# Kernel optimization log

Measured on AMD Instinct MI355X. Metric: run time of the kernel, lower is better.

The kernel has to match this reference:

```python
import jax, jax.numpy as jnp
import numpy as np

D_MODEL = 1024
N_HEAD = 16


def setup_inputs() -> dict:
    key = jax.random.key(0)
    kx, kw = jax.random.split(key)
    x = jax.random.normal(kx, (4, 2048, D_MODEL), dtype=jnp.float32)
    # fused QKV projection weight, torch Linear: y = x @ W.T, W: [3*d_model, d_model]
    W_qkv = jax.random.normal(kw, (3 * D_MODEL, D_MODEL), dtype=jnp.float32) * (D_MODEL ** -0.5)
    return {"x": x, "W_qkv": W_qkv}


def reference(x, W_qkv):
    B, T, C = x.shape
    hd = C // N_HEAD
    qkv = jnp.einsum('btc,fc->btf', x, W_qkv)  # [B,T,3C]
    q, k, v = jnp.split(qkv, 3, axis=-1)
    # [B, H, T, hd]
    q = q.reshape(B, T, N_HEAD, hd).transpose(0, 2, 1, 3)
    k = k.reshape(B, T, N_HEAD, hd).transpose(0, 2, 1, 3)
    v = v.reshape(B, T, N_HEAD, hd).transpose(0, 2, 1, 3)
    scale = 1.0 / jnp.sqrt(jnp.asarray(hd, dtype=x.dtype))
    scores = jnp.einsum('bhqd,bhkd->bhqk', q, k) * scale  # [B,H,T,T]
    causal = jnp.tril(jnp.ones((T, T), dtype=bool))
    scores = jnp.where(causal, scores, jnp.asarray(-jnp.inf, dtype=scores.dtype))
    w = jax.nn.softmax(scores, axis=-1)
    out = jnp.einsum('bhqk,bhkd->bhqd', w, v)  # [B,H,T,hd]
    return out
```

## Files before the change

kernel.cpp:

```cpp
#include <hip/hip_runtime.h>
#include <hip/hip_bf16.h>
#include <math.h>

#define D_MODEL 1024
#define N_HEAD  16
#define HD      64
#define B_SZ    4
#define T_SEQ   2048
#define M_TOT   (B_SZ * T_SEQ)
#define N_TOT   (3 * D_MODEL)

typedef __bf16 bf16_t;
typedef __bf16 bf16x8 __attribute__((ext_vector_type(8)));
typedef __bf16 bf16x4 __attribute__((ext_vector_type(4)));
typedef __bf16 bf16x2 __attribute__((ext_vector_type(2)));
typedef float  f32x4  __attribute__((ext_vector_type(4)));
typedef float  f32x16 __attribute__((ext_vector_type(16)));
typedef int    i32x4  __attribute__((ext_vector_type(4)));

#define Q_PRESCALE 0.18033688011112042f

__global__ __launch_bounds__(256) void cvt_f32_bf16(const float* __restrict__ in,
                                                    bf16_t* __restrict__ out, int n4) {
  int i = blockIdx.x * blockDim.x + threadIdx.x;
  int stride = gridDim.x * blockDim.x;
  for (; i < n4; i += stride) {
    float4 v = ((const float4*)in)[i];
    bf16x4 o;
    o[0] = (bf16_t)v.x; o[1] = (bf16_t)v.y; o[2] = (bf16_t)v.z; o[3] = (bf16_t)v.w;
    ((bf16x4*)out)[i] = o;
  }
}

__global__ __launch_bounds__(256) void qkv_gemm(const bf16_t* __restrict__ xb,
                                                const bf16_t* __restrict__ wb,
                                                bf16_t* __restrict__ Q,
                                                bf16_t* __restrict__ Kf,
                                                bf16_t* __restrict__ Vf) {
  __shared__ alignas(16) bf16_t smem[24576];
  bf16_t* a_lds = smem;
  bf16_t* b_lds = smem + 12288;
  bf16_t* c_lds = smem;

  const int tid  = threadIdx.x;
  const int wave = tid >> 6;
  const int lane = tid & 63;
  const int bm = blockIdx.y * 128;
  const int bn = blockIdx.x * 128;
  const int sec = bn >> 10;

  f32x4 acc[4][4] = {};

  const int sRow  = lane >> 2;
  const int sCol8 = (lane & 3) ^ ((lane >> 3) & 3);
  const int fr = lane & 15;
  const int fk = lane >> 4;
  const int wm = (wave >> 1) * 64;
  const int wn = (wave & 1) * 64;

  auto stage = [&](int buf, int kk) {
#pragma unroll
    for (int c = 0; c < 2; ++c) {
      const int chunk = wave * 2 + c;
      const bf16_t* gA = &xb[(size_t)(bm + chunk * 16 + sRow) * D_MODEL + kk + sCol8 * 8];
      __builtin_amdgcn_global_load_lds(
          (__attribute__((address_space(1))) void*)(void*)gA,
          (__attribute__((address_space(3))) void*)&a_lds[buf * 4096 + chunk * 512], 16, 0, 0);
      const bf16_t* gB = &wb[(size_t)(bn + chunk * 16 + sRow) * D_MODEL + kk + sCol8 * 8];
      __builtin_amdgcn_global_load_lds(
          (__attribute__((address_space(1))) void*)(void*)gB,
          (__attribute__((address_space(3))) void*)&b_lds[buf * 4096 + chunk * 512], 16, 0, 0);
    }
  };

  auto loadFrags = [&](int buf, bf16x8 af[4], bf16x8 bfr[4]) {
#pragma unroll
    for (int mt = 0; mt < 4; ++mt) {
      const int row = wm + mt * 16 + fr;
      af[mt] = *(const bf16x8*)&a_lds[buf * 4096 + row * 32 + (fk ^ ((fr >> 1) & 3)) * 8];
    }
#pragma unroll
    for (int nt = 0; nt < 4; ++nt) {
      const int row = wn + nt * 16 + fr;
      bfr[nt] = *(const bf16x8*)&b_lds[buf * 4096 + row * 32 + (fk ^ ((fr >> 1) & 3)) * 8];
    }
  };

  auto mfmaAll = [&](bf16x8 af[4], bf16x8 bfr[4]) {
    __builtin_amdgcn_s_setprio(1);
#pragma unroll
    for (int mt = 0; mt < 4; ++mt)
#pragma unroll
      for (int nt = 0; nt < 4; ++nt)
        acc[mt][nt] = __builtin_amdgcn_mfma_f32_16x16x32_bf16(af[mt], bfr[nt], acc[mt][nt], 0, 0, 0);
    __builtin_amdgcn_s_setprio(0);
  };

  stage(0, 0);
  stage(1, 32);
  int cur = 0;
  for (int t = 0; t < 31; ++t) {
    asm volatile("s_waitcnt vmcnt(4)" ::: "memory");
    __builtin_amdgcn_s_barrier();
    __builtin_amdgcn_sched_barrier(0);
    bf16x8 af[4], bfr[4];
    loadFrags(cur, af, bfr);
    if (t < 30) stage((t + 2) % 3, (t + 2) * 32);
    mfmaAll(af, bfr);
    cur = (cur + 1) % 3;
  }
  asm volatile("s_waitcnt vmcnt(0)" ::: "memory");
  __builtin_amdgcn_s_barrier();
  __builtin_amdgcn_sched_barrier(0);
  {
    bf16x8 af[4], bfr[4];
    loadFrags(cur, af, bfr);
    mfmaAll(af, bfr);
  }

  const int cRowBase = (lane >> 4) * 4;
  const int cCol     = lane & 15;

  if (sec == 2) {
#pragma unroll
    for (int mt = 0; mt < 4; ++mt) {
#pragma unroll
      for (int nt = 0; nt < 4; ++nt) {
        const int hn = (bn & 1023) + wn + nt * 16 + cCol;
        const int h  = hn >> 6;
        const int d  = hn & 63;
        const int mbase = bm + wm + mt * 16 + cRowBase;
        const int b  = mbase >> 11;
        const int t0 = mbase & 2047;
        const int kvt = t0 >> 5, tt0 = t0 & 31;
        const int idx = (d >> 5) * 2 + (tt0 >> 4);
        const int h2  = (tt0 >> 3) & 1;
        const int j0  = tt0 & 7;
        bf16x4 pk;
        pk[0] = (bf16_t)acc[mt][nt][0]; pk[1] = (bf16_t)acc[mt][nt][1];
        pk[2] = (bf16_t)acc[mt][nt][2]; pk[3] = (bf16_t)acc[mt][nt][3];
        const size_t bhOff = (size_t)(b * N_HEAD + h) * (T_SEQ * HD);
        *(bf16x4*)&Vf[bhOff + (size_t)(((kvt * 4 + idx) * 64 + h2 * 32 + (d & 31)) * 8 + j0)] = pk;
      }
    }
  } else {
    __syncthreads();
    const float qs = (sec == 0) ? Q_PRESCALE : 1.0f;
#pragma unroll
    for (int mt = 0; mt < 4; ++mt)
#pragma unroll
      for (int nt = 0; nt < 4; ++nt)
#pragma unroll
        for (int r = 0; r < 4; ++r) {
          const int mloc = wm + mt * 16 + cRowBase + r;
          const int nloc = wn + nt * 16 + cCol;
          c_lds[mloc * 132 + nloc] = (bf16_t)(acc[mt][nt][r] * qs);
        }
    __syncthreads();

    const int row = tid >> 1;
    const int nh  = tid & 1;
    const int m = bm + row;
    const int b = m >> 11, t = m & 2047;
    const int h = ((bn & 1023) + nh * 64) >> 6;
    const size_t bhOff = (size_t)(b * N_HEAD + h) * (T_SEQ * HD);

    if (sec == 0) {
      bf16_t* qp = Q + bhOff + (size_t)t * HD;
#pragma unroll
      for (int o = 0; o < 16; ++o) {
        bf16x4 vv = *(const bf16x4*)&c_lds[row * 132 + nh * 64 + o * 4];
        *(bf16x4*)&qp[o * 4] = vv;
      }
    } else {
      const int kvt = t >> 5, lk = t & 31;
#pragma unroll
      for (int o = 0; o < 16; ++o) {
        const int d0 = o * 4;
        const int cc = d0 >> 4, h2 = (d0 >> 3) & 1, j0 = d0 & 7;
        bf16x4 vv = *(const bf16x4*)&c_lds[row * 132 + nh * 64 + d0];
        *(bf16x4*)&Kf[bhOff + (size_t)(((kvt * 4 + cc) * 64 + h2 * 32 + lk) * 8 + j0)] = vv;
      }
    }
  }
}

__device__ inline int pack_bf16(float lo, float hi) {
  bf16x2 v; v[0] = (bf16_t)lo; v[1] = (bf16_t)hi;
  return __builtin_bit_cast(int, v);
}
__device__ inline void permswap(int& a, int& b) {
  asm volatile("v_permlane32_swap_b32 %0, %1" : "+v"(a), "+v"(b));
}
__device__ inline void loadK4(bf16x8 k[4], const bf16_t* __restrict__ Kbase,
                              int kv0, int lane) {
  const bf16_t* p = Kbase + (size_t)(kv0 >> 5) * 2048 + lane * 8;
#pragma unroll
  for (int c = 0; c < 4; ++c) k[c] = *(const bf16x8*)(p + c * 512);
}
__device__ inline void loadV4(bf16x8 v[4], const bf16_t* __restrict__ Vbase,
                              int kv0, int lane) {
  const bf16_t* p = Vbase + (size_t)(kv0 >> 5) * 2048 + lane * 8;
#pragma unroll
  for (int idx = 0; idx < 4; ++idx) v[idx] = *(const bf16x8*)(p + idx * 512);
}

__global__ __launch_bounds__(256, 4) void attn_fwd(const bf16_t* __restrict__ Q,
                                                   const bf16_t* __restrict__ Kf,
                                                   const bf16_t* __restrict__ Vf,
                                                   float* __restrict__ out) {
  __shared__ float o_sh[2][64][33];
  __shared__ float m_sh[2][32];
  __shared__ float l_sh[2][32];

  const int tid  = threadIdx.x;
  const int wave = tid >> 6;
  const int lane = tid & 63;
  const int l31  = lane & 31;
  const int hi   = lane >> 5;

  const int f   = blockIdx.x;
  const int bh  = ((f & 7) << 3) | ((f >> 3) & 7);
  const int pr  = f >> 6;
  const int grp = wave >> 1;
  const int isWriter = wave & 1;
  const int chunk = grp ? (63 - pr) : pr;
  const int q0 = chunk * 32;
  const int n  = chunk + 1;
  const int h  = (n + 1) >> 1;
  const int j0 = isWriter ? h : 0;
  const int j1 = isWriter ? n : h;

  const bf16_t* Qp = Q  + (size_t)bh * T_SEQ * HD;
  const bf16_t* Kp = Kf + (size_t)bh * T_SEQ * HD;
  const bf16_t* Vp = Vf + (size_t)bh * T_SEQ * HD;
  float* op = out + (size_t)bh * T_SEQ * HD;

  bf16x8 qf[4];
#pragma unroll
  for (int c = 0; c < 4; ++c)
    qf[c] = *(const bf16x8*)&Qp[(size_t)(q0 + l31) * HD + c * 16 + hi * 8];

  f32x16 o0 = {}, o1 = {};
  float m_run = -INFINITY;
  float l_run = 0.f;

  if (j0 < j1) {
    bf16x8 kA[4], vA[4];
    loadK4(kA, Kp, j0 * 32, lane);

    for (int j = j0; j < j1; ++j) {
      const int kv0 = j * 32;
      loadV4(vA, Vp, kv0, lane);

      f32x16 st = {};
      __builtin_amdgcn_s_setprio(1);
#pragma unroll
      for (int c = 0; c < 4; ++c)
        st = __builtin_amdgcn_mfma_f32_32x32x16_bf16(kA[c], qf[c], st, 0, 0, 0);
      __builtin_amdgcn_s_setprio(0);

      const int nxt = (j + 1 < j1) ? (j + 1) * 32 : kv0;
      loadK4(kA, Kp, nxt, lane);

      if (kv0 == q0) {
#pragma unroll
        for (int r = 0; r < 16; ++r) {
          const int koff = (r & 3) + 8 * (r >> 2) + 4 * hi;
          st[r] = (koff > l31) ? -INFINITY : st[r];
        }
      }
      float pm = fmaxf(fmaxf(fmaxf(st[0], st[1]), fmaxf(st[2], st[3])),
                       fmaxf(fmaxf(st[4], st[5]), fmaxf(st[6], st[7])));
      pm = fmaxf(pm, fmaxf(fmaxf(fmaxf(st[8], st[9]), fmaxf(st[10], st[11])),
                           fmaxf(fmaxf(st[12], st[13]), fmaxf(st[14], st[15]))));

      if (__any(!(pm <= m_run + 8.f))) {
        const float pm_full = fmaxf(pm, __shfl_xor(pm, 32));
        const float m_new = fmaxf(m_run, pm_full);
        const float alpha = exp2f(m_run - m_new);
        m_run = m_new;
        l_run *= alpha;
#pragma unroll
        for (int r = 0; r < 16; ++r) {
          const int qr = (r & 3) + 8 * (r >> 2) + 4 * hi;
          const float av = __shfl(alpha, qr);
          o0[r] *= av; o1[r] *= av;
        }
      }

      float p[16];
#pragma unroll
      for (int r = 0; r < 16; ++r) p[r] = exp2f(st[r] - m_run);
      float s0 = (p[0] + p[1]) + (p[2] + p[3]);
      float s1 = (p[4] + p[5]) + (p[6] + p[7]);
      float s2 = (p[8] + p[9]) + (p[10] + p[11]);
      float s3 = (p[12] + p[13]) + (p[14] + p[15]);
      l_run += (s0 + s1) + (s2 + s3);

      int a01 = pack_bf16(p[0],  p[1]),  a23 = pack_bf16(p[2],  p[3]);
      int b01 = pack_bf16(p[4],  p[5]),  b23 = pack_bf16(p[6],  p[7]);
      int c01 = pack_bf16(p[8],  p[9]),  c23 = pack_bf16(p[10], p[11]);
      int d01 = pack_bf16(p[12], p[13]), d23 = pack_bf16(p[14], p[15]);
      permswap(a01, b01); permswap(a23, b23);
      permswap(c01, d01); permswap(c23, d23);
      i32x4 w1 = {a01, a23, b01, b23};
      i32x4 w2 = {c01, c23, d01, d23};
      bf16x8 f1 = __builtin_bit_cast(bf16x8, w1);
      bf16x8 f2 = __builtin_bit_cast(bf16x8, w2);

      __builtin_amdgcn_s_setprio(1);
      o0 = __builtin_amdgcn_mfma_f32_32x32x16_bf16(f1, vA[0], o0, 0, 0, 0);
      o0 = __builtin_amdgcn_mfma_f32_32x32x16_bf16(f2, vA[1], o0, 0, 0, 0);
      o1 = __builtin_amdgcn_mfma_f32_32x32x16_bf16(f1, vA[2], o1, 0, 0, 0);
      o1 = __builtin_amdgcn_mfma_f32_32x32x16_bf16(f2, vA[3], o1, 0, 0, 0);
      __builtin_amdgcn_s_setprio(0);
    }
  }

  const float l_comb = l_run + __shfl_xor(l_run, 32);

  if (isWriter) {
#pragma unroll
    for (int r = 0; r < 16; ++r) {
      o_sh[grp][lane][r]      = o0[r];
      o_sh[grp][lane][16 + r] = o1[r];
    }
    if (lane < 32) {
      m_sh[grp][lane] = m_run;
      l_sh[grp][lane] = l_comb;
    }
  }
  __syncthreads();
  if (!isWriter) {
#pragma unroll
    for (int r = 0; r < 16; ++r) {
      const int qr = (r & 3) + 8 * (r >> 2) + 4 * hi;
      const float mB = m_sh[grp][qr];
      const float lB = l_sh[grp][qr];
      const float mA = __shfl(m_run, qr);
      const float lA = __shfl(l_comb, qr);
      const float mM = fmaxf(mA, mB);
      const float aA = exp2f(mA - mM);
      const float aB = exp2f(mB - mM);
      const float li = 1.f / (lA * aA + lB * aB);
      const float x0 = (o0[r] * aA + o_sh[grp][lane][r]      * aB) * li;
      const float x1 = (o1[r] * aA + o_sh[grp][lane][16 + r] * aB) * li;
      op[(size_t)(q0 + qr) * HD + l31]      = x0;
      op[(size_t)(q0 + qr) * HD + 32 + l31] = x1;
    }
  }
}

extern "C" void kernel_launch(void* const* d_in, const int* in_sizes, int n_in,
                              void* d_out, int out_size, void* d_ws, size_t ws_size,
                              hipStream_t stream) {
  const float* x = (const float*)d_in[0];
  const float* W = (const float*)d_in[1];
  float* out = (float*)d_out;

  char* ws = (char*)d_ws;
  bf16_t* xb  = (bf16_t*)(ws);
  bf16_t* wb  = (bf16_t*)(ws + 16777216);
  bf16_t* Qb  = (bf16_t*)(ws + 16777216 + 6291456);
  bf16_t* Kfb = Qb + 8388608;
  bf16_t* Vfb = Kfb + 8388608;

  cvt_f32_bf16<<<2048, 256, 0, stream>>>(x, xb, (M_TOT * D_MODEL) / 4);
  cvt_f32_bf16<<<1024, 256, 0, stream>>>(W, wb, (N_TOT * D_MODEL) / 4);

  dim3 ggrid(N_TOT / 128, M_TOT / 128);
  qkv_gemm<<<ggrid, 256, 0, stream>>>(xb, wb, Qb, Kfb, Vfb);

  attn_fwd<<<2048, 256, 0, stream>>>(Qb, Kfb, Vfb, out);
}
```

Measured before the change: 151.3 us.

## Split each query chunk's KV range across four waves instead of pairing chunks

Each attention block previously took two mirrored query chunks (pr and 63-pr), and two waves split each chunk's KV range in half. Now each block handles a single query chunk, and all four waves each take a quarter of the KV tiles. Wave 0 merges the other three waves' partial outputs using the online-softmax rescaling, and the grid doubles to 4096 blocks. This is meant to shorten each wave's serial KV loop and rely on the block scheduler for load balance. In exchange it adds a larger four-way LDS reduction, leaves waves idle on short early chunks, and drops the explicit pairing that balanced work per block.

```diff
diff --git a/kernel.cpp b/kernel.cpp
--- a/kernel.cpp
+++ b/kernel.cpp
@@ -209,9 +209,9 @@
                                                    const bf16_t* __restrict__ Kf,
                                                    const bf16_t* __restrict__ Vf,
                                                    float* __restrict__ out) {
-  __shared__ float o_sh[2][64][33];
-  __shared__ float m_sh[2][32];
-  __shared__ float l_sh[2][32];
+  __shared__ float o_sh[3][64][33];
+  __shared__ float m_sh[3][32];
+  __shared__ float l_sh[3][32];
 
   const int tid  = threadIdx.x;
   const int wave = tid >> 6;
@@ -219,17 +219,14 @@
   const int l31  = lane & 31;
   const int hi   = lane >> 5;
 
-  const int f   = blockIdx.x;
-  const int bh  = ((f & 7) << 3) | ((f >> 3) & 7);
-  const int pr  = f >> 6;
-  const int grp = wave >> 1;
-  const int isWriter = wave & 1;
-  const int chunk = grp ? (63 - pr) : pr;
+  const int f     = blockIdx.x;
+  const int bh    = ((f & 7) << 3) | ((f >> 3) & 7);
+  const int chunk = f >> 6;
   const int q0 = chunk * 32;
   const int n  = chunk + 1;
-  const int h  = (n + 1) >> 1;
-  const int j0 = isWriter ? h : 0;
-  const int j1 = isWriter ? n : h;
+  const int s  = (n + 3) >> 2;
+  const int j0 = wave * s;
+  const int j1 = min(j0 + s, n);
 
   const bf16_t* Qp = Q  + (size_t)bh * T_SEQ * HD;
   const bf16_t* Kp = Kf + (size_t)bh * T_SEQ * HD;
@@ -320,32 +317,35 @@
 
   const float l_comb = l_run + __shfl_xor(l_run, 32);
 
-  if (isWriter) {
+  if (wave != 0) {
+    const int slot = wave - 1;
 #pragma unroll
     for (int r = 0; r < 16; ++r) {
-      o_sh[grp][lane][r]      = o0[r];
-      o_sh[grp][lane][16 + r] = o1[r];
+      o_sh[slot][lane][r]      = o0[r];
+      o_sh[slot][lane][16 + r] = o1[r];
     }
     if (lane < 32) {
-      m_sh[grp][lane] = m_run;
-      l_sh[grp][lane] = l_comb;
+      m_sh[slot][lane] = m_run;
+      l_sh[slot][lane] = l_comb;
     }
   }
   __syncthreads();
-  if (!isWriter) {
+  if (wave == 0) {
 #pragma unroll
     for (int r = 0; r < 16; ++r) {
       const int qr = (r & 3) + 8 * (r >> 2) + 4 * hi;
-      const float mB = m_sh[grp][qr];
-      const float lB = l_sh[grp][qr];
       const float mA = __shfl(m_run, qr);
       const float lA = __shfl(l_comb, qr);
-      const float mM = fmaxf(mA, mB);
-      const float aA = exp2f(mA - mM);
-      const float aB = exp2f(mB - mM);
-      const float li = 1.f / (lA * aA + lB * aB);
-      const float x0 = (o0[r] * aA + o_sh[grp][lane][r]      * aB) * li;
-      const float x1 = (o1[r] * aA + o_sh[grp][lane][16 + r] * aB) * li;
+      const float m1 = m_sh[0][qr], m2 = m_sh[1][qr], m3 = m_sh[2][qr];
+      const float l1 = l_sh[0][qr], l2 = l_sh[1][qr], l3 = l_sh[2][qr];
+      const float mM = fmaxf(fmaxf(mA, m1), fmaxf(m2, m3));
+      const float a0 = exp2f(mA - mM), a1 = exp2f(m1 - mM);
+      const float a2 = exp2f(m2 - mM), a3 = exp2f(m3 - mM);
+      const float li = 1.f / (lA * a0 + l1 * a1 + l2 * a2 + l3 * a3);
+      const float x0 = (o0[r] * a0 + o_sh[0][lane][r] * a1 +
+                        o_sh[1][lane][r] * a2 + o_sh[2][lane][r] * a3) * li;
+      const float x1 = (o1[r] * a0 + o_sh[0][lane][16 + r] * a1 +
+                        o_sh[1][lane][16 + r] * a2 + o_sh[2][lane][16 + r] * a3) * li;
       op[(size_t)(q0 + qr) * HD + l31]      = x0;
       op[(size_t)(q0 + qr) * HD + 32 + l31] = x1;
     }
@@ -372,5 +372,5 @@
   dim3 ggrid(N_TOT / 128, M_TOT / 128);
   qkv_gemm<<<ggrid, 256, 0, stream>>>(xb, wb, Qb, Kfb, Vfb);
 
-  attn_fwd<<<2048, 256, 0, stream>>>(Qb, Kfb, Vfb, out);
-}
+  attn_fwd<<<4096, 256, 0, stream>>>(Qb, Kfb, Vfb, out);
+}
```

After: 154.8 us. 2.3% more time.
